# Optimization experiments

Hardware: AMD Instinct MI355X
Metric: run time of the kernel (lower is better)

Reference implementation:

```python
import jax, jax.numpy as jnp
import numpy as np

DIM = 768
HID = 24576          # hidden_features (SAE dictionary size)
DENSE = 3072         # dense_hidden_features (MLP width)
NUM_LAYERS = 12
L = NUM_LAYERS * 2   # forward requires x.shape[1] == num_layers*2 (broadcast with decoder_b2)
B = 64
K = 16               # num_active_features


def setup_inputs() -> dict:
    key = jax.random.key(0)
    ks = jax.random.split(key, 10)
    s1 = 1.0 / np.sqrt(DIM)
    s2 = 1.0 / np.sqrt(DENSE)
    s3 = 1.0 / np.sqrt(HID)
    return {
        "x": jax.random.normal(ks[0], (B, L, DIM), dtype=jnp.float32),
        "encoder_w1": jax.random.uniform(ks[1], (DENSE, DIM), jnp.float32, -s1, s1),
        "encoder_b1": jnp.zeros((DENSE,), jnp.float32),
        "encoder_w2": jax.random.uniform(ks[2], (HID, DENSE), jnp.float32, -s2, s2),
        "encoder_b2": jnp.zeros((HID,), jnp.float32),
        "decoder_w1": jax.random.uniform(ks[3], (DENSE, HID), jnp.float32, -s3, s3),
        "decoder_b1": jnp.zeros((DENSE,), jnp.float32),
        "decoder_w2": jax.random.uniform(ks[4], (DIM, DENSE), jnp.float32, -s2, s2),
        "decoder_b2": jax.random.uniform(ks[5], (1, L, DIM), jnp.float32, -s1, s1),
    }


def reference(x, encoder_w1, encoder_b1, encoder_w2, encoder_b2,
              decoder_w1, decoder_b1, decoder_w2, decoder_b2):
    # subtract per-(layer,dim) decoder bias, dense encode, GELU (exact, matches nn.GELU)
    h = jax.nn.gelu(jnp.einsum('blc,dc->bld', x - decoder_b2, encoder_w1) + encoder_b1,
                    approximate=False)                         # [B, L, DENSE]
    z = jnp.einsum('bld,nd->bln', h, encoder_w2) + encoder_b2  # [B, L, HID]
    # topk mask: keep only K largest per (b, l), zero the rest (scatter of ones)
    _, idx = jax.lax.top_k(z, K)                               # [B, L, K]
    b_idx = jnp.arange(z.shape[0])[:, None, None]
    l_idx = jnp.arange(z.shape[1])[None, :, None]
    mask = jnp.zeros_like(z).at[b_idx, l_idx, idx].set(1.0)
    z = jax.nn.relu(z * mask)                                  # act_fn = ReLU
    # dense decode (full GEMM over mostly-zero hidden dim, as in the original)
    d = jax.nn.gelu(jnp.einsum('bln,dn->bld', z, decoder_w1) + decoder_b1,
                    approximate=False)                         # [B, L, DENSE]
    return jnp.einsum('bld,cd->blc', d, decoder_w2) + decoder_b2  # [B, L, DIM]
```

## Files before the change

kernel.cpp:

```cpp
#include <hip/hip_runtime.h>
#include <hip/hip_fp16.h>

#define DIM 768
#define HID 24576
#define DENSE 3072
#define LL 24
#define MROWS 1536
#define KSEL 16
#define NC 24
#define CAP 40
#define MF_TOT 96
#define ENC2_NT 96
#define DELTA 2e-3f

typedef _Float16 f16;
typedef __attribute__((ext_vector_type(8))) _Float16 f16x8;
typedef __attribute__((ext_vector_type(4))) float f32x4;
typedef const __attribute__((address_space(1))) char* gcp;
typedef __attribute__((address_space(3))) char* lcp;

__device__ __forceinline__ float gelu_exact(float x) {
    return 0.5f * x * (1.0f + erff(x * 0.7071067811865476f));
}

__device__ __forceinline__ void split8(const float4& v0, const float4& v1,
                                       f16x8& hi, f16x8& lo) {
    float vv[8] = {v0.x, v0.y, v0.z, v0.w, v1.x, v1.y, v1.z, v1.w};
#pragma unroll
    for (int j = 0; j < 8; ++j) {
        f16 h = (f16)vv[j];
        hi[j] = h;
        lo[j] = (f16)((vv[j] - (float)h) * 2048.0f);
    }
}


template <int KTOT, int RFTOT>
__global__ __launch_bounds__(256) void apack_kernel(
    const float* __restrict__ src, f16* __restrict__ dst) {
    int c = blockIdx.x * 4 + (threadIdx.x >> 6);
    int lane = threadIdx.x & 63;
    int rf = c % RFTOT, ks = c / RFTOT;
    int m = rf * 16 + (lane & 15);
    int k = ks * 32 + (lane >> 4) * 8;
    const float4* s = (const float4*)(src + (size_t)m * (KTOT * 32) + k);
    f16x8 hi, lo;
    split8(s[0], s[1], hi, lo);
    char* base = (char*)dst + (size_t)c * 2048 + lane * 16;
    *(f16x8*)base = hi;
    *(f16x8*)(base + 1024) = lo;
}

__global__ __launch_bounds__(256) void xcpack_kernel(
    const float* __restrict__ x, const float* __restrict__ b2,
    f16* __restrict__ dst) {
    int c = blockIdx.x * 4 + (threadIdx.x >> 6);
    int lane = threadIdx.x & 63;
    int rf = c % MF_TOT, ks = c / MF_TOT;
    int m = rf * 16 + (lane & 15);
    int k = ks * 32 + (lane >> 4) * 8;
    const float4* sx = (const float4*)(x + (size_t)m * DIM + k);
    const float4* sb = (const float4*)(b2 + (m % LL) * DIM + k);
    float4 v0 = sx[0], v1 = sx[1], b0 = sb[0], b1 = sb[1];
    v0.x -= b0.x; v0.y -= b0.y; v0.z -= b0.z; v0.w -= b0.w;
    v1.x -= b1.x; v1.y -= b1.y; v1.z -= b1.z; v1.w -= b1.w;
    f16x8 hi, lo;
    split8(v0, v1, hi, lo);
    char* base = (char*)dst + (size_t)c * 2048 + lane * 16;
    *(f16x8*)base = hi;
    *(f16x8*)(base + 1024) = lo;
}

template <int KTOT>
__global__ __launch_bounds__(256) void wpack_kernel(
    const float* __restrict__ src, f16* __restrict__ dst, int row0) {
    int c = blockIdx.x * 4 + (threadIdx.x >> 6);
    int lane = threadIdx.x & 63;
    int nf = c & 7; int t = c >> 3; int ks = t % KTOT; int nb = t / KTOT;
    int n = row0 + nb * 128 + nf * 16 + (lane & 15);
    int k = ks * 32 + (lane >> 4) * 8;
    const float4* s = (const float4*)(src + (size_t)n * (KTOT * 32) + k);
    f16x8 hi, lo;
    split8(s[0], s[1], hi, lo);
    char* base = (char*)dst + (size_t)c * 2048 + lane * 16;
    *(f16x8*)base = hi;
    *(f16x8*)(base + 1024) = lo;
}

__global__ __launch_bounds__(256) void apackhi_kernel(
    const float* __restrict__ src, f16* __restrict__ dst) {
    int c = blockIdx.x * 4 + (threadIdx.x >> 6);
    int lane = threadIdx.x & 63;
    int rf = c % MF_TOT, ks = c / MF_TOT;
    int m = rf * 16 + (lane & 15);
    int k = ks * 32 + (lane >> 4) * 8;
    const float4* s = (const float4*)(src + (size_t)m * DENSE + k);
    float4 v0 = s[0], v1 = s[1];
    float vv[8] = {v0.x, v0.y, v0.z, v0.w, v1.x, v1.y, v1.z, v1.w};
    f16x8 hi;
#pragma unroll
    for (int j = 0; j < 8; ++j) hi[j] = (f16)vv[j];
    *(f16x8*)((char*)dst + (size_t)c * 1024 + lane * 16) = hi;
}

__global__ __launch_bounds__(256) void wpackhi_kernel(
    const float* __restrict__ src, f16* __restrict__ dst) {
    int c = blockIdx.x * 4 + (threadIdx.x >> 6);
    int lane = threadIdx.x & 63;
    int nf = c & 7; int t = c >> 3; int ks = t % 96; int nb = t / 96;
    int n = nb * 128 + nf * 16 + (lane & 15);
    int k = ks * 32 + (lane >> 4) * 8;
    const float4* s = (const float4*)(src + (size_t)n * DENSE + k);
    float4 v0 = s[0], v1 = s[1];
    float vv[8] = {v0.x, v0.y, v0.z, v0.w, v1.x, v1.y, v1.z, v1.w};
    f16x8 hi;
#pragma unroll
    for (int j = 0; j < 8; ++j) hi[j] = (f16)vv[j];
    *(f16x8*)((char*)dst + (size_t)c * 1024 + lane * 16) = hi;
}

__global__ __launch_bounds__(256) void transpose_w1_kernel(
    const float* __restrict__ src, __half* __restrict__ dst) {
    __shared__ float tile[32][33];
    const int c0 = blockIdx.x * 32;
    const int r0 = blockIdx.y * 32;
    const int tx = threadIdx.x & 31, ty = threadIdx.x >> 5;
#pragma unroll
    for (int i = 0; i < 32; i += 8)
        tile[ty + i][tx] = src[(size_t)(r0 + ty + i) * HID + c0 + tx];
    __syncthreads();
#pragma unroll
    for (int i = 0; i < 32; i += 8)
        dst[(size_t)(c0 + ty + i) * DENSE + r0 + tx] = __float2half(tile[tx][ty + i]);
}

template <int KTOT, int EPI>
__global__ __launch_bounds__(256, 2) void mfma_nt_kernel(
    const f16* __restrict__ Apk, const f16* __restrict__ Wpk,
    const float* __restrict__ bias, float* __restrict__ C,
    int N, int n0g) {
    __shared__ __align__(16) char lds[2][32768];
    const int tid = threadIdx.x;
    const int lane = tid & 63, wave = tid >> 6;
    const int mb = blockIdx.x, nb = blockIdx.y;
    const int wr = wave >> 1, wc = wave & 1;
    const char* ApkB = (const char*)Apk;
    const char* WpkB = (const char*)Wpk;

    f32x4 accH[4][4] = {}; f32x4 accL[4][4] = {};

    auto stage = [&](int buf, int ks) {
        const char* Ar = ApkB + (size_t)(ks * MF_TOT + mb * 8) * 2048;
        const char* Wr = WpkB + (size_t)(nb * KTOT + ks) * 16384;
#pragma unroll
        for (int q = 0; q < 8; ++q) {
            int c = wave * 8 + q;
            const char* src = (c < 16 ? Ar + c * 1024 : Wr + (c - 16) * 1024) + lane * 16;
            char* dst = &lds[buf][c * 1024];
            __builtin_amdgcn_global_load_lds((gcp)src, (lcp)dst, 16, 0, 0);
        }
    };

    stage(0, 0);
    for (int ks = 0; ks < KTOT; ++ks) {
        int cur = ks & 1;
        __syncthreads();
        if (ks + 1 < KTOT) stage(cur ^ 1, ks + 1);
        const char* Bf = lds[cur];
        f16x8 Ahi[4], Alo[4], Whi[4], Wlo[4];
#pragma unroll
        for (int i = 0; i < 4; ++i) {
            Ahi[i] = *(const f16x8*)(Bf + ((wr * 4 + i) * 2 + 0) * 1024 + lane * 16);
            Alo[i] = *(const f16x8*)(Bf + ((wr * 4 + i) * 2 + 1) * 1024 + lane * 16);
            Whi[i] = *(const f16x8*)(Bf + 16384 + ((wc * 4 + i) * 2 + 0) * 1024 + lane * 16);
            Wlo[i] = *(const f16x8*)(Bf + 16384 + ((wc * 4 + i) * 2 + 1) * 1024 + lane * 16);
        }
#pragma unroll
        for (int i = 0; i < 4; ++i)
#pragma unroll
            for (int j = 0; j < 4; ++j) {
                accH[i][j] = __builtin_amdgcn_mfma_f32_16x16x32_f16(Ahi[i], Whi[j], accH[i][j], 0, 0, 0);
                accL[i][j] = __builtin_amdgcn_mfma_f32_16x16x32_f16(Ahi[i], Wlo[j], accL[i][j], 0, 0, 0);
                accL[i][j] = __builtin_amdgcn_mfma_f32_16x16x32_f16(Alo[i], Whi[j], accL[i][j], 0, 0, 0);
            }
    }
    const int rbase = mb * 128 + wr * 64 + (lane >> 4) * 4;
    const int cb = n0g + nb * 128 + wc * 64 + (lane & 15);
#pragma unroll
    for (int j = 0; j < 4; ++j) {
        int col = cb + j * 16;
        float bn = (EPI == 2) ? 0.0f : bias[col];
#pragma unroll
        for (int i = 0; i < 4; ++i) {
#pragma unroll
            for (int e = 0; e < 4; ++e) {
                int row = rbase + i * 16 + e;
                float v = accH[i][j][e] + accL[i][j][e] * (1.0f / 2048.0f);
                if (EPI == 1)       v = gelu_exact(v + bn);
                else if (EPI == 0)  v += bn;
                else                v += bias[(row % LL) * N + col];
                C[(size_t)row * N + col] = v;
            }
        }
    }
}

__global__ __launch_bounds__(512, 4) void enc2v3_kernel(
    const f16* __restrict__ Apk, const f16* __restrict__ Wpk,
    const float* __restrict__ b2, __half* __restrict__ z) {
    __shared__ __align__(16) char lds[3][24576];
    const int tid = threadIdx.x;
    const int lane = tid & 63, wave = tid >> 6;
    int f = blockIdx.y * 6 + blockIdx.x;
    int ff = (f & 7) * 144 + (f >> 3);
    const int mb = ff % 6, nb = ff / 6;
    const int wr = wave >> 1, wc = wave & 1;
    const char* ApkB = (const char*)Apk;
    const char* WpkB = (const char*)Wpk;
    f32x4 acc[4][4] = {};

    auto stage = [&](int t) {
        if (t >= ENC2_NT) return;
        char* dst = lds[t % 3];
        const char* Asrc = ApkB + ((size_t)t * MF_TOT + mb * 16) * 1024;
        __builtin_amdgcn_global_load_lds((gcp)(Asrc + tid * 16),
                                         (lcp)(dst + (tid & ~63) * 16), 16, 0, 0);
        __builtin_amdgcn_global_load_lds((gcp)(Asrc + tid * 16 + 8192),
                                         (lcp)(dst + (tid & ~63) * 16 + 8192), 16, 0, 0);
        const char* Wsrc = WpkB + ((size_t)nb * 96 + t) * 8192;
        __builtin_amdgcn_global_load_lds((gcp)(Wsrc + tid * 16),
                                         (lcp)(dst + 16384 + (tid & ~63) * 16), 16, 0, 0);
    };

    stage(0); stage(1);
    asm volatile("s_waitcnt vmcnt(3)" ::: "memory");
    __builtin_amdgcn_s_barrier();

    for (int t = 0; t < ENC2_NT; ++t) {
        const char* Bf = lds[t % 3];
        f16x8 Af[4], Wf[4];
#pragma unroll
        for (int i = 0; i < 4; ++i) {
            Af[i] = *(const f16x8*)(Bf + (wr * 4 + i) * 1024 + lane * 16);
            Wf[i] = *(const f16x8*)(Bf + 16384 + (wc * 4 + i) * 1024 + lane * 16);
        }
        stage(t + 2);
        __builtin_amdgcn_s_setprio(1);
#pragma unroll
        for (int i = 0; i < 4; ++i)
#pragma unroll
            for (int j = 0; j < 4; ++j)
                acc[i][j] = __builtin_amdgcn_mfma_f32_16x16x32_f16(Af[i], Wf[j], acc[i][j], 0, 0, 0);
        __builtin_amdgcn_s_setprio(0);
        if (t < ENC2_NT - 2)      asm volatile("s_waitcnt vmcnt(3)" ::: "memory");
        else if (t < ENC2_NT - 1) asm volatile("s_waitcnt vmcnt(0)" ::: "memory");
        if (t < ENC2_NT - 1) __builtin_amdgcn_s_barrier();
    }
    const int rbase = mb * 256 + wr * 64 + (lane >> 4) * 4;
    const int cb = nb * 128 + wc * 64 + (lane & 15);
#pragma unroll
    for (int j = 0; j < 4; ++j) {
        int col = cb + j * 16;
        float bn = b2[col];
#pragma unroll
        for (int r = 0; r < 4; ++r)
#pragma unroll
            for (int e = 0; e < 4; ++e)
                z[(size_t)(rbase + r * 16 + e) * HID + col] = __float2half(acc[r][j][e] + bn);
    }
}

__global__ __launch_bounds__(512) void topksel_kernel(
    const __half* __restrict__ z, int* __restrict__ candi, int* __restrict__ candn) {
    __shared__ unsigned short keys[HID];
    __shared__ unsigned hist[256];
    __shared__ int sB1, sA, sT, scnt;
    const int row = blockIdx.x, tid = threadIdx.x;
    const int lane = tid & 63, wave = tid >> 6;
    const uint4* zr = reinterpret_cast<const uint4*>(z + (size_t)row * HID);
    if (tid < 256) hist[tid] = 0;
    if (tid == 0) scnt = 0;
    __syncthreads();
#pragma unroll
    for (int i = 0; i < 6; ++i) {
        uint4 v = zr[tid + i * 512];
        unsigned w[4] = {v.x, v.y, v.z, v.w};
        int base = (tid + i * 512) * 8;
#pragma unroll
        for (int q = 0; q < 4; ++q)
#pragma unroll
            for (int s = 0; s < 2; ++s) {
                unsigned b = (w[q] >> (16 * s)) & 0xFFFFu;
                unsigned kk = b ^ ((b & 0x8000u) ? 0xFFFFu : 0x8000u);
                keys[base + q * 2 + s] = (unsigned short)kk;
                atomicAdd(&hist[kk >> 8], 1u);
            }
    }
    __syncthreads();
    if (wave == 0) {
        const int b0 = 252 - 4 * lane;
        int part = 0;
#pragma unroll
        for (int j = 0; j < 4; ++j) part += (int)hist[b0 + j];
        int incl = part;
#pragma unroll
        for (int off = 1; off < 64; off <<= 1) {
            int v = __shfl_up(incl, off);
            if (lane >= off) incl += v;
        }
        int pre = incl - part;
        if (pre < NC && NC <= incl) {
            int cum = pre;
            for (int j = 3; j >= 0; --j) {
                int hh = (int)hist[b0 + j];
                if (cum + hh >= NC) { sB1 = b0 + j; sA = cum; break; }
                cum += hh;
            }
        }
    }
    __syncthreads();
    const int B1 = sB1, t2 = NC - sA;
    __syncthreads();
    if (tid < 256) hist[tid] = 0;
    __syncthreads();
#pragma unroll
    for (int i = 0; i < 48; ++i) {
        unsigned kk = keys[tid + i * 512];
        if ((int)(kk >> 8) == B1) atomicAdd(&hist[kk & 0xFF], 1u);
    }
    __syncthreads();
    if (wave == 0) {
        const int b0 = 252 - 4 * lane;
        int part = 0;
#pragma unroll
        for (int j = 0; j < 4; ++j) part += (int)hist[b0 + j];
        int incl = part;
#pragma unroll
        for (int off = 1; off < 64; off <<= 1) {
            int v = __shfl_up(incl, off);
            if (lane >= off) incl += v;
        }
        int pre = incl - part;
        if (pre < t2 && t2 <= incl) {
            int cum = pre;
            for (int j = 3; j >= 0; --j) {
                int hh = (int)hist[b0 + j];
                if (cum + hh >= t2) { sT = (B1 << 8) | (b0 + j); break; }
                cum += hh;
            }
        }
    }
    __syncthreads();
    const unsigned T = (unsigned)sT;
#pragma unroll
    for (int i = 0; i < 48; ++i) {
        int idx = tid + i * 512;
        if ((unsigned)keys[idx] >= T) {
            int p = atomicAdd(&scnt, 1);
            if (p < CAP) candi[(size_t)row * CAP + p] = idx;
        }
    }
    __syncthreads();
    if (tid == 0) candn[row] = min(scnt, CAP);
}

__global__ __launch_bounds__(256) void resolve16_kernel(
    const __half* __restrict__ z, const float* __restrict__ h,
    const float* __restrict__ w2, const float* __restrict__ b2,
    const int* __restrict__ candi, const int* __restrict__ candn,
    float* __restrict__ tkv, int* __restrict__ tki) {
    const int row = blockIdx.x, tid = threadIdx.x;
    const int lane = tid & 63, wave = tid >> 6;
    __shared__ float hs[DENSE];
    __shared__ float av[64];
    __shared__ int ci[64];
    __shared__ int bnd[CAP];
    __shared__ int nb_s;
    const int cnt = candn[row];
    const float4* hr = reinterpret_cast<const float4*>(h + (size_t)row * DENSE);
#pragma unroll
    for (int j = 0; j < 3; ++j)
        reinterpret_cast<float4*>(hs)[tid + j * 256] = hr[tid + j * 256];
    if (wave == 0) {
        float myv = -1e30f;
        int myi = 0x7fffffff;
        if (lane < cnt) {
            myi = candi[(size_t)row * CAP + lane];
            myv = __half2float(z[(size_t)row * HID + myi]);
        }
        int rank = 0;
#pragma unroll
        for (int o = 0; o < CAP; ++o) {
            float ov = __shfl(myv, o);
            int oi = __shfl(myi, o);
            rank += ((ov > myv) || (ov == myv && oi < myi)) ? 1 : 0;
        }
        unsigned long long m15 = __ballot(rank == 15);
        int sl = (int)__builtin_ctzll(m15);
        float v16 = __shfl(myv, sl);
        bool band = (lane < cnt) && (fabsf(myv - v16) <= DELTA);
        unsigned long long bm = __ballot(band);
        if (lane == 0) nb_s = (int)__popcll(bm);
        if (band) {
            int p = (int)__popcll(bm & ((1ull << lane) - 1ull));
            bnd[p] = lane;
        }
        av[lane] = myv;
        ci[lane] = myi;
    }
    __syncthreads();
    const int nbn = nb_s;
    for (int b = wave; b < nbn; b += 4) {
        int c = bnd[b];
        int n = ci[c];
        const float4* wr = reinterpret_cast<const float4*>(w2 + (size_t)n * DENSE);
        float p = 0.0f;
#pragma unroll
        for (int j = 0; j < 12; ++j) {
            float4 a = reinterpret_cast<const float4*>(hs)[lane + j * 64];
            float4 w = wr[lane + j * 64];
            p += a.x * w.x + a.y * w.y + a.z * w.z + a.w * w.w;
        }
#pragma unroll
        for (int off = 32; off >= 1; off >>= 1) p += __shfl_down(p, off);
        if (lane == 0) av[c] = p + b2[n];
    }
    __syncthreads();
    if (wave == 0) {
        float v = av[lane];
        int idx = ci[lane];
        int rank = 0;
#pragma unroll
        for (int o = 0; o < CAP; ++o) {
            float ov = __shfl(v, o);
            int oi = __shfl(idx, o);
            rank += ((ov > v) || (ov == v && oi < idx)) ? 1 : 0;
        }
        if (lane < cnt && rank < KSEL) {
            tkv[row * KSEL + rank] = fmaxf(v, 0.0f);
            tki[row * KSEL + rank] = idx;
        }
    }
}

__global__ __launch_bounds__(256) void sparse_decode_kernel(
    const float* __restrict__ tkv, const int* __restrict__ tki,
    const __half* __restrict__ w1t, const float* __restrict__ b1,
    float* __restrict__ D) {
    const int row = blockIdx.x, tid = threadIdx.x;
    __shared__ float sv[KSEL];
    __shared__ int si[KSEL];
    if (tid < KSEL) { sv[tid] = tkv[row * KSEL + tid]; si[tid] = tki[row * KSEL + tid]; }
    __syncthreads();
    float2 acc[6] = {};
#pragma unroll 1
    for (int k = 0; k < KSEL; ++k) {
        const float v = sv[k];
        const __half2* wr = reinterpret_cast<const __half2*>(w1t + (size_t)si[k] * DENSE);
#pragma unroll
        for (int j = 0; j < 6; ++j) {
            float2 f = __half22float2(wr[tid + j * 256]);
            acc[j].x = fmaf(v, f.x, acc[j].x);
            acc[j].y = fmaf(v, f.y, acc[j].y);
        }
    }
#pragma unroll
    for (int j = 0; j < 6; ++j) {
        int dd = (tid + j * 256) * 2;
        D[(size_t)row * DENSE + dd]     = gelu_exact(acc[j].x + b1[dd]);
        D[(size_t)row * DENSE + dd + 1] = gelu_exact(acc[j].y + b1[dd + 1]);
    }
}

extern "C" void kernel_launch(void* const* d_in, const int* in_sizes, int n_in,
                              void* d_out, int out_size, void* d_ws, size_t ws_size,
                              hipStream_t stream) {
    const float* x      = (const float*)d_in[0];
    const float* enc_w1 = (const float*)d_in[1];
    const float* enc_b1 = (const float*)d_in[2];
    const float* enc_w2 = (const float*)d_in[3];
    const float* enc_b2 = (const float*)d_in[4];
    const float* dec_w1 = (const float*)d_in[5];
    const float* dec_b1 = (const float*)d_in[6];
    const float* dec_w2 = (const float*)d_in[7];
    const float* dec_b2 = (const float*)d_in[8];
    float* out = (float*)d_out;

    char* ws = (char*)d_ws;
    size_t off = 0;
    f16*    Wpk = (f16*)(ws + off);
    __half* w1t = (__half*)(ws + off); off += (size_t)HID * DENSE * 2;
    __half* z    = (__half*)(ws + off); off += (size_t)MROWS * HID * 2;
    f16*    ApkHi = (f16*)(ws + off);  off += (size_t)MROWS * DENSE * 2;
    f16*    Dpk  = (f16*)(ws + off);   off += (size_t)MROWS * DENSE * 4;
    float*  h    = (float*)(ws + off); off += (size_t)MROWS * DENSE * 4;
    float*  dbuf = (float*)(ws + off); off += (size_t)MROWS * DENSE * 4;
    f16*    W1pk = (f16*)(ws + off);
    f16*    Wd2pk = (f16*)(ws + off);  off += (size_t)DENSE * DIM * 4;
    f16*    xcpk = (f16*)(ws + off);   off += (size_t)MROWS * DIM * 4;
    float*  tkv  = (float*)(ws + off); off += (size_t)MROWS * KSEL * 4;
    int*    tki  = (int*)(ws + off);   off += (size_t)MROWS * KSEL * 4;
    int*    candi = (int*)(ws + off);  off += (size_t)MROWS * CAP * 4;
    int*    candn = (int*)(ws + off);  off += (size_t)MROWS * 4;

    xcpack_kernel<<<24 * MF_TOT / 4, 256, 0, stream>>>(x, dec_b2, xcpk);
    wpack_kernel<24><<<24 * 24 * 8 / 4, 256, 0, stream>>>(enc_w1, W1pk, 0);
    mfma_nt_kernel<24, 1><<<dim3(12, 24), 256, 0, stream>>>(
        xcpk, W1pk, enc_b1, h, DENSE, 0);
    apackhi_kernel<<<96 * MF_TOT / 4, 256, 0, stream>>>(h, ApkHi);
    wpackhi_kernel<<<192 * 96 * 8 / 4, 256, 0, stream>>>(enc_w2, Wpk);
    enc2v3_kernel<<<dim3(6, 192), 512, 0, stream>>>(ApkHi, Wpk, enc_b2, z);
    transpose_w1_kernel<<<dim3(HID / 32, DENSE / 32), 256, 0, stream>>>(dec_w1, w1t);
    topksel_kernel<<<MROWS, 512, 0, stream>>>(z, candi, candn);
    resolve16_kernel<<<MROWS, 256, 0, stream>>>(
        z, h, enc_w2, enc_b2, candi, candn, tkv, tki);
    sparse_decode_kernel<<<MROWS, 256, 0, stream>>>(tkv, tki, w1t, dec_b1, dbuf);
    apack_kernel<96, 96><<<96 * 96 / 4, 256, 0, stream>>>(dbuf, Dpk);
    wpack_kernel<96><<<6 * 96 * 8 / 4, 256, 0, stream>>>(dec_w2, Wd2pk, 0);
    mfma_nt_kernel<96, 2><<<dim3(12, 6), 256, 0, stream>>>(
        Dpk, Wd2pk, dec_b2, out, DIM, 0);
}
```

Before: 623.4 us.

## Merge pack kernels, add 64x64 decode GEMM, replicate topk histograms, vectorize decode

Pairs of independent packing kernels are merged into single launches (prep1, prep2) to cut launch overhead. The final decode GEMM moves from 128x128 tiles on 72 blocks to a new 64x64-tile kernel on 288 blocks so more CUs are busy. The topk histogram is replicated four ways to reduce LDS atomic contention, and the sparse decode reads and writes 4-wide vectors. The smaller GEMM tiles lower data reuse per block, and the replicated histograms cost extra LDS and extra summing work.

```diff
diff --git a/kernel.cpp b/kernel.cpp
--- a/kernel.cpp
+++ b/kernel.cpp
@@ -51,24 +51,38 @@
     *(f16x8*)(base + 1024) = lo;
 }
 
-__global__ __launch_bounds__(256) void xcpack_kernel(
+__global__ __launch_bounds__(256) void prep1_kernel(
     const float* __restrict__ x, const float* __restrict__ b2,
-    f16* __restrict__ dst) {
-    int c = blockIdx.x * 4 + (threadIdx.x >> 6);
+    f16* __restrict__ xcpk,
+    const float* __restrict__ w1src, f16* __restrict__ W1pk) {
     int lane = threadIdx.x & 63;
-    int rf = c % MF_TOT, ks = c / MF_TOT;
-    int m = rf * 16 + (lane & 15);
-    int k = ks * 32 + (lane >> 4) * 8;
-    const float4* sx = (const float4*)(x + (size_t)m * DIM + k);
-    const float4* sb = (const float4*)(b2 + (m % LL) * DIM + k);
-    float4 v0 = sx[0], v1 = sx[1], b0 = sb[0], b1 = sb[1];
-    v0.x -= b0.x; v0.y -= b0.y; v0.z -= b0.z; v0.w -= b0.w;
-    v1.x -= b1.x; v1.y -= b1.y; v1.z -= b1.z; v1.w -= b1.w;
-    f16x8 hi, lo;
-    split8(v0, v1, hi, lo);
-    char* base = (char*)dst + (size_t)c * 2048 + lane * 16;
-    *(f16x8*)base = hi;
-    *(f16x8*)(base + 1024) = lo;
+    if (blockIdx.x < 576) {
+        int c = blockIdx.x * 4 + (threadIdx.x >> 6);
+        int rf = c % MF_TOT, ks = c / MF_TOT;
+        int m = rf * 16 + (lane & 15);
+        int k = ks * 32 + (lane >> 4) * 8;
+        const float4* sx = (const float4*)(x + (size_t)m * DIM + k);
+        const float4* sb = (const float4*)(b2 + (m % LL) * DIM + k);
+        float4 v0 = sx[0], v1 = sx[1], b0 = sb[0], b1 = sb[1];
+        v0.x -= b0.x; v0.y -= b0.y; v0.z -= b0.z; v0.w -= b0.w;
+        v1.x -= b1.x; v1.y -= b1.y; v1.z -= b1.z; v1.w -= b1.w;
+        f16x8 hi, lo;
+        split8(v0, v1, hi, lo);
+        char* base = (char*)xcpk + (size_t)c * 2048 + lane * 16;
+        *(f16x8*)base = hi;
+        *(f16x8*)(base + 1024) = lo;
+    } else {
+        int c = (blockIdx.x - 576) * 4 + (threadIdx.x >> 6);
+        int nf = c & 7; int t = c >> 3; int ks = t % 24; int nb = t / 24;
+        int n = nb * 128 + nf * 16 + (lane & 15);
+        int k = ks * 32 + (lane >> 4) * 8;
+        const float4* s = (const float4*)(w1src + (size_t)n * DIM + k);
+        f16x8 hi, lo;
+        split8(s[0], s[1], hi, lo);
+        char* base = (char*)W1pk + (size_t)c * 2048 + lane * 16;
+        *(f16x8*)base = hi;
+        *(f16x8*)(base + 1024) = lo;
+    }
 }
 
 template <int KTOT>
@@ -87,36 +101,35 @@
     *(f16x8*)(base + 1024) = lo;
 }
 
-__global__ __launch_bounds__(256) void apackhi_kernel(
-    const float* __restrict__ src, f16* __restrict__ dst) {
-    int c = blockIdx.x * 4 + (threadIdx.x >> 6);
+__global__ __launch_bounds__(256) void prep2_kernel(
+    const float* __restrict__ h, f16* __restrict__ ApkHi,
+    const float* __restrict__ w2, f16* __restrict__ Wpk) {
     int lane = threadIdx.x & 63;
-    int rf = c % MF_TOT, ks = c / MF_TOT;
-    int m = rf * 16 + (lane & 15);
-    int k = ks * 32 + (lane >> 4) * 8;
-    const float4* s = (const float4*)(src + (size_t)m * DENSE + k);
-    float4 v0 = s[0], v1 = s[1];
-    float vv[8] = {v0.x, v0.y, v0.z, v0.w, v1.x, v1.y, v1.z, v1.w};
-    f16x8 hi;
-#pragma unroll
-    for (int j = 0; j < 8; ++j) hi[j] = (f16)vv[j];
-    *(f16x8*)((char*)dst + (size_t)c * 1024 + lane * 16) = hi;
-}
-
-__global__ __launch_bounds__(256) void wpackhi_kernel(
-    const float* __restrict__ src, f16* __restrict__ dst) {
-    int c = blockIdx.x * 4 + (threadIdx.x >> 6);
-    int lane = threadIdx.x & 63;
-    int nf = c & 7; int t = c >> 3; int ks = t % 96; int nb = t / 96;
-    int n = nb * 128 + nf * 16 + (lane & 15);
-    int k = ks * 32 + (lane >> 4) * 8;
-    const float4* s = (const float4*)(src + (size_t)n * DENSE + k);
-    float4 v0 = s[0], v1 = s[1];
-    float vv[8] = {v0.x, v0.y, v0.z, v0.w, v1.x, v1.y, v1.z, v1.w};
-    f16x8 hi;
-#pragma unroll
-    for (int j = 0; j < 8; ++j) hi[j] = (f16)vv[j];
-    *(f16x8*)((char*)dst + (size_t)c * 1024 + lane * 16) = hi;
+    if (blockIdx.x < 2304) {
+        int c = blockIdx.x * 4 + (threadIdx.x >> 6);
+        int rf = c % MF_TOT, ks = c / MF_TOT;
+        int m = rf * 16 + (lane & 15);
+        int k = ks * 32 + (lane >> 4) * 8;
+        const float4* s = (const float4*)(h + (size_t)m * DENSE + k);
+        float4 v0 = s[0], v1 = s[1];
+        float vv[8] = {v0.x, v0.y, v0.z, v0.w, v1.x, v1.y, v1.z, v1.w};
+        f16x8 hi;
+#pragma unroll
+        for (int j = 0; j < 8; ++j) hi[j] = (f16)vv[j];
+        *(f16x8*)((char*)ApkHi + (size_t)c * 1024 + lane * 16) = hi;
+    } else {
+        int c = (blockIdx.x - 2304) * 4 + (threadIdx.x >> 6);
+        int nf = c & 7; int t = c >> 3; int ks = t % 96; int nb = t / 96;
+        int n = nb * 128 + nf * 16 + (lane & 15);
+        int k = ks * 32 + (lane >> 4) * 8;
+        const float4* s = (const float4*)(w2 + (size_t)n * DENSE + k);
+        float4 v0 = s[0], v1 = s[1];
+        float vv[8] = {v0.x, v0.y, v0.z, v0.w, v1.x, v1.y, v1.z, v1.w};
+        f16x8 hi;
+#pragma unroll
+        for (int j = 0; j < 8; ++j) hi[j] = (f16)vv[j];
+        *(f16x8*)((char*)Wpk + (size_t)c * 1024 + lane * 16) = hi;
+    }
 }
 
 __global__ __launch_bounds__(256) void transpose_w1_kernel(
@@ -200,6 +213,74 @@
                 else if (EPI == 0)  v += bn;
                 else                v += bias[(row % LL) * N + col];
                 C[(size_t)row * N + col] = v;
+            }
+        }
+    }
+}
+
+__global__ __launch_bounds__(256, 4) void mfma64_kernel(
+    const f16* __restrict__ Apk, const f16* __restrict__ Wpk,
+    const float* __restrict__ bias, float* __restrict__ C) {
+    __shared__ __align__(16) char lds[2][16384];
+    const int tid = threadIdx.x;
+    const int lane = tid & 63, wave = tid >> 6;
+    const int mb = blockIdx.x, nbi = blockIdx.y;
+    const int wr = wave >> 1, wc = wave & 1;
+    const char* ApkB = (const char*)Apk;
+    const char* WpkB = (const char*)Wpk;
+
+    f32x4 accH[2][2] = {}; f32x4 accL[2][2] = {};
+
+    auto stage = [&](int buf, int ks) {
+        const char* Ar = ApkB + (size_t)(ks * 96 + mb * 4) * 2048;
+        const char* Wr = WpkB + (((size_t)(nbi >> 1) * 96 + ks) * 8 + (nbi & 1) * 4) * 2048;
+#pragma unroll
+        for (int q = 0; q < 2; ++q) {
+            __builtin_amdgcn_global_load_lds(
+                (gcp)(Ar + tid * 16 + q * 4096),
+                (lcp)(&lds[buf][0] + (tid & ~63) * 16 + q * 4096), 16, 0, 0);
+            __builtin_amdgcn_global_load_lds(
+                (gcp)(Wr + tid * 16 + q * 4096),
+                (lcp)(&lds[buf][8192] + (tid & ~63) * 16 + q * 4096), 16, 0, 0);
+        }
+    };
+
+    stage(0, 0);
+    for (int ks = 0; ks < 96; ++ks) {
+        int cur = ks & 1;
+        __syncthreads();
+        if (ks + 1 < 96) stage(cur ^ 1, ks + 1);
+        const char* Bf = lds[cur];
+        f16x8 Ahi[2], Alo[2], Whi[2], Wlo[2];
+#pragma unroll
+        for (int i = 0; i < 2; ++i) {
+            Ahi[i] = *(const f16x8*)(Bf + (wr * 2 + i) * 2048 + lane * 16);
+            Alo[i] = *(const f16x8*)(Bf + (wr * 2 + i) * 2048 + 1024 + lane * 16);
+            Whi[i] = *(const f16x8*)(Bf + 8192 + (wc * 2 + i) * 2048 + lane * 16);
+            Wlo[i] = *(const f16x8*)(Bf + 8192 + (wc * 2 + i) * 2048 + 1024 + lane * 16);
+        }
+#pragma unroll
+        for (int i = 0; i < 2; ++i)
+#pragma unroll
+            for (int j = 0; j < 2; ++j) {
+                accH[i][j] = __builtin_amdgcn_mfma_f32_16x16x32_f16(Ahi[i], Whi[j], accH[i][j], 0, 0, 0);
+                accL[i][j] = __builtin_amdgcn_mfma_f32_16x16x32_f16(Ahi[i], Wlo[j], accL[i][j], 0, 0, 0);
+                accL[i][j] = __builtin_amdgcn_mfma_f32_16x16x32_f16(Alo[i], Whi[j], accL[i][j], 0, 0, 0);
+            }
+    }
+    const int rbase = mb * 64 + wr * 32 + (lane >> 4) * 4;
+    const int cb = nbi * 64 + wc * 32 + (lane & 15);
+#pragma unroll
+    for (int j = 0; j < 2; ++j) {
+        int col = cb + j * 16;
+#pragma unroll
+        for (int i = 0; i < 2; ++i) {
+#pragma unroll
+            for (int e = 0; e < 4; ++e) {
+                int row = rbase + i * 16 + e;
+                float v = accH[i][j][e] + accL[i][j][e] * (1.0f / 2048.0f)
+                        + bias[(row % LL) * DIM + col];
+                C[(size_t)row * DIM + col] = v;
             }
         }
     }
@@ -273,12 +354,13 @@
 __global__ __launch_bounds__(512) void topksel_kernel(
     const __half* __restrict__ z, int* __restrict__ candi, int* __restrict__ candn) {
     __shared__ unsigned short keys[HID];
-    __shared__ unsigned hist[256];
+    __shared__ unsigned hist[4][256];
     __shared__ int sB1, sA, sT, scnt;
     const int row = blockIdx.x, tid = threadIdx.x;
     const int lane = tid & 63, wave = tid >> 6;
+    const int hrep = wave & 3;
     const uint4* zr = reinterpret_cast<const uint4*>(z + (size_t)row * HID);
-    if (tid < 256) hist[tid] = 0;
+    if (tid < 256) { hist[0][tid] = 0; hist[1][tid] = 0; hist[2][tid] = 0; hist[3][tid] = 0; }
     if (tid == 0) scnt = 0;
     __syncthreads();
 #pragma unroll
@@ -293,15 +375,17 @@
                 unsigned b = (w[q] >> (16 * s)) & 0xFFFFu;
                 unsigned kk = b ^ ((b & 0x8000u) ? 0xFFFFu : 0x8000u);
                 keys[base + q * 2 + s] = (unsigned short)kk;
-                atomicAdd(&hist[kk >> 8], 1u);
+                atomicAdd(&hist[hrep][kk >> 8], 1u);
             }
     }
     __syncthreads();
     if (wave == 0) {
         const int b0 = 252 - 4 * lane;
-        int part = 0;
-#pragma unroll
-        for (int j = 0; j < 4; ++j) part += (int)hist[b0 + j];
+        int bc[4];
+#pragma unroll
+        for (int j = 0; j < 4; ++j)
+            bc[j] = (int)(hist[0][b0 + j] + hist[1][b0 + j] + hist[2][b0 + j] + hist[3][b0 + j]);
+        int part = bc[0] + bc[1] + bc[2] + bc[3];
         int incl = part;
 #pragma unroll
         for (int off = 1; off < 64; off <<= 1) {
@@ -312,28 +396,29 @@
         if (pre < NC && NC <= incl) {
             int cum = pre;
             for (int j = 3; j >= 0; --j) {
-                int hh = (int)hist[b0 + j];
-                if (cum + hh >= NC) { sB1 = b0 + j; sA = cum; break; }
-                cum += hh;
+                if (cum + bc[j] >= NC) { sB1 = b0 + j; sA = cum; break; }
+                cum += bc[j];
             }
         }
     }
     __syncthreads();
     const int B1 = sB1, t2 = NC - sA;
     __syncthreads();
-    if (tid < 256) hist[tid] = 0;
+    if (tid < 256) { hist[0][tid] = 0; hist[1][tid] = 0; hist[2][tid] = 0; hist[3][tid] = 0; }
     __syncthreads();
 #pragma unroll
     for (int i = 0; i < 48; ++i) {
         unsigned kk = keys[tid + i * 512];
-        if ((int)(kk >> 8) == B1) atomicAdd(&hist[kk & 0xFF], 1u);
+        if ((int)(kk >> 8) == B1) atomicAdd(&hist[hrep][kk & 0xFF], 1u);
     }
     __syncthreads();
     if (wave == 0) {
         const int b0 = 252 - 4 * lane;
-        int part = 0;
-#pragma unroll
-        for (int j = 0; j < 4; ++j) part += (int)hist[b0 + j];
+        int bc[4];
+#pragma unroll
+        for (int j = 0; j < 4; ++j)
+            bc[j] = (int)(hist[0][b0 + j] + hist[1][b0 + j] + hist[2][b0 + j] + hist[3][b0 + j]);
+        int part = bc[0] + bc[1] + bc[2] + bc[3];
         int incl = part;
 #pragma unroll
         for (int off = 1; off < 64; off <<= 1) {
@@ -344,9 +429,8 @@
         if (pre < t2 && t2 <= incl) {
             int cum = pre;
             for (int j = 3; j >= 0; --j) {
-                int hh = (int)hist[b0 + j];
-                if (cum + hh >= t2) { sT = (B1 << 8) | (b0 + j); break; }
-                cum += hh;
+                if (cum + bc[j] >= t2) { sT = (B1 << 8) | (b0 + j); break; }
+                cum += bc[j];
             }
         }
     }
@@ -452,23 +536,31 @@
     __shared__ int si[KSEL];
     if (tid < KSEL) { sv[tid] = tkv[row * KSEL + tid]; si[tid] = tki[row * KSEL + tid]; }
     __syncthreads();
-    float2 acc[6] = {};
+    float acc[3][4] = {};
 #pragma unroll 1
     for (int k = 0; k < KSEL; ++k) {
         const float v = sv[k];
-        const __half2* wr = reinterpret_cast<const __half2*>(w1t + (size_t)si[k] * DENSE);
-#pragma unroll
-        for (int j = 0; j < 6; ++j) {
-            float2 f = __half22float2(wr[tid + j * 256]);
-            acc[j].x = fmaf(v, f.x, acc[j].x);
-            acc[j].y = fmaf(v, f.y, acc[j].y);
-        }
-    }
-#pragma unroll
-    for (int j = 0; j < 6; ++j) {
-        int dd = (tid + j * 256) * 2;
-        D[(size_t)row * DENSE + dd]     = gelu_exact(acc[j].x + b1[dd]);
-        D[(size_t)row * DENSE + dd + 1] = gelu_exact(acc[j].y + b1[dd + 1]);
+        const uint2* wr = reinterpret_cast<const uint2*>(w1t + (size_t)si[k] * DENSE);
+#pragma unroll
+        for (int j = 0; j < 3; ++j) {
+            uint2 u = wr[tid + j * 256];
+            float2 f0 = __half22float2(*reinterpret_cast<const __half2*>(&u.x));
+            float2 f1 = __half22float2(*reinterpret_cast<const __half2*>(&u.y));
+            acc[j][0] = fmaf(v, f0.x, acc[j][0]);
+            acc[j][1] = fmaf(v, f0.y, acc[j][1]);
+            acc[j][2] = fmaf(v, f1.x, acc[j][2]);
+            acc[j][3] = fmaf(v, f1.y, acc[j][3]);
+        }
+    }
+#pragma unroll
+    for (int j = 0; j < 3; ++j) {
+        int dd = (tid + j * 256) * 4;
+        float4 o;
+        o.x = gelu_exact(acc[j][0] + b1[dd]);
+        o.y = gelu_exact(acc[j][1] + b1[dd + 1]);
+        o.z = gelu_exact(acc[j][2] + b1[dd + 2]);
+        o.w = gelu_exact(acc[j][3] + b1[dd + 3]);
+        *reinterpret_cast<float4*>(D + (size_t)row * DENSE + dd) = o;
     }
 }
 
@@ -503,12 +595,10 @@
     int*    candi = (int*)(ws + off);  off += (size_t)MROWS * CAP * 4;
     int*    candn = (int*)(ws + off);  off += (size_t)MROWS * 4;
 
-    xcpack_kernel<<<24 * MF_TOT / 4, 256, 0, stream>>>(x, dec_b2, xcpk);
-    wpack_kernel<24><<<24 * 24 * 8 / 4, 256, 0, stream>>>(enc_w1, W1pk, 0);
+    prep1_kernel<<<576 + 1152, 256, 0, stream>>>(x, dec_b2, xcpk, enc_w1, W1pk);
     mfma_nt_kernel<24, 1><<<dim3(12, 24), 256, 0, stream>>>(
         xcpk, W1pk, enc_b1, h, DENSE, 0);
-    apackhi_kernel<<<96 * MF_TOT / 4, 256, 0, stream>>>(h, ApkHi);
-    wpackhi_kernel<<<192 * 96 * 8 / 4, 256, 0, stream>>>(enc_w2, Wpk);
+    prep2_kernel<<<2304 + 36864, 256, 0, stream>>>(h, ApkHi, enc_w2, Wpk);
     enc2v3_kernel<<<dim3(6, 192), 512, 0, stream>>>(ApkHi, Wpk, enc_b2, z);
     transpose_w1_kernel<<<dim3(HID / 32, DENSE / 32), 256, 0, stream>>>(dec_w1, w1t);
     topksel_kernel<<<MROWS, 512, 0, stream>>>(z, candi, candn);
@@ -517,6 +607,5 @@
     sparse_decode_kernel<<<MROWS, 256, 0, stream>>>(tkv, tki, w1t, dec_b1, dbuf);
     apack_kernel<96, 96><<<96 * 96 / 4, 256, 0, stream>>>(dbuf, Dpk);
     wpack_kernel<96><<<6 * 96 * 8 / 4, 256, 0, stream>>>(dec_w2, Wd2pk, 0);
-    mfma_nt_kernel<96, 2><<<dim3(12, 6), 256, 0, stream>>>(
-        Dpk, Wd2pk, dec_b2, out, DIM, 0);
-}
+    mfma64_kernel<<<dim3(24, 12), 256, 0, stream>>>(Dpk, Wd2pk, dec_b2, out);
+}
```

Result: faster. 587.8 us (-5.7%).
